# Performance work log

Measured on AMD Instinct MI355X. Metric: run time of the kernel, lower is better.

Reference implementation:

```python
import jax, jax.numpy as jnp
import numpy as np

N, L2, C = 4096, 49, 128   # lmax=6 -> (lmax+1)**2 = 49
RES = 18                   # grid resolution (beta, alpha)


def setup_inputs() -> dict:
    key = jax.random.key(0)
    k1, k2, k3 = jax.random.split(key, 3)
    inputs = jax.random.normal(k1, (N, L2, C), dtype=jnp.float32)
    # Stand-ins for the precomputed spherical-harmonic transform matrices
    # (to_grid_mat / from_grid_mat), shape (res_beta, res_alpha, (lmax+1)**2).
    W_to = jax.random.normal(k2, (RES, RES, L2), dtype=jnp.float32) / jnp.sqrt(jnp.float32(L2))
    W_from = jax.random.normal(k3, (RES, RES, L2), dtype=jnp.float32) / jnp.sqrt(jnp.float32(RES * RES))
    return {"inputs": inputs, "W_to": W_to, "W_from": W_from}


def reference(inputs, W_to, W_from):
    # to_grid: coefficients -> real-space S2 grid  (n, beta, alpha, c)
    grid = jnp.einsum('bai,nic->nbac', W_to, inputs)
    # elementwise self tensor product on the grid
    grid = grid * grid
    # from_grid: project back to spherical-harmonic coefficients (n, i, c)
    outputs = jnp.einsum('bai,nbac->nic', W_from, grid)
    return outputs
```

## Files before the change

### kernel.cpp

```cpp
#include <hip/hip_runtime.h>


#define NN    4096
#define L2D   49
#define CCH   128
#define GTOT  324
#define MT1P  22
#define KC2   11

typedef __attribute__((ext_vector_type(8))) short bf16x8;
typedef __attribute__((ext_vector_type(4))) float f32x4;

#define WT_SHORTS (MT1P * 2 * 64 * 8)
#define WF_SHORTS (4 * KC2 * 64 * 8)
#define W_SHORTS  (WT_SHORTS + WF_SHORTS)

__device__ __forceinline__ short f2bf(float f) {
    union { float f; unsigned u; } x; x.f = f;
    return (short)((x.u + 0x7fffu + ((x.u >> 16) & 1u)) >> 16);
}

__device__ __forceinline__ unsigned cvtpk(float lo, float hi) {
    unsigned r;
    asm("v_cvt_pk_bf16_f32 %0, %1, %2" : "=v"(r) : "v"(lo), "v"(hi));
    return r;
}

__global__ void prep_w_kernel(const float* __restrict__ Wt,
                              const float* __restrict__ Wf,
                              short* __restrict__ WtF,
                              short* __restrict__ WfF)
{
    int idx = blockIdx.x * 256 + threadIdx.x;
    if (idx < WT_SHORTS) {
        int j = idx & 7, lane = (idx >> 3) & 63, kcx = (idx >> 9) & 1, mt = idx >> 10;
        int g = mt * 16 + (lane & 15);
        int i = kcx * 32 + (lane >> 4) * 8 + j;
        WtF[idx] = f2bf((g < GTOT && i < L2D) ? Wt[g * L2D + i] : 0.0f);
    } else if (idx < WT_SHORTS + WF_SHORTS) {
        int e = idx - WT_SHORTS;
        int j = e & 7, lane = (e >> 3) & 63, t = e >> 9;
        int kc2 = t % KC2, it = t / KC2;
        int i = it * 16 + (lane & 15);
        int g = kc2 * 32 + (j >> 2) * 16 + (lane >> 4) * 4 + (j & 3);
        WfF[e] = f2bf((g < GTOT && i < L2D) ? Wf[g * L2D + i] : 0.0f);
    }
}

__global__ __launch_bounds__(1024, 4)
void stp_mfma3_kernel(const float* __restrict__ inp,
                      const short* __restrict__ Wbase,
                      float* __restrict__ out)
{
    __shared__ __attribute__((aligned(16))) short sW[W_SHORTS];

    const int tid = threadIdx.x;

    {
        const uint4* __restrict__ src = (const uint4*)Wbase;
        uint4* dst = (uint4*)sW;
        #pragma unroll
        for (int e = 0; e < 6; ++e) {
            int idx = tid + e * 1024;
            if (idx < W_SHORTS / 8) dst[idx] = src[idx];
        }
    }
    __syncthreads();

    const int lane = tid & 63;
    const int wave = tid >> 6;
    const int lm   = lane & 15;
    const int quad = lane >> 4;
    const int q    = wave & 3;
    const int nw   = wave >> 2;

    const short* sWt = sW;
    const short* sWf = sW + WT_SHORTS;

    for (int rep = 0; rep < 4; ++rep) {
        const int n = blockIdx.x * 16 + rep * 4 + nw;
        const float* __restrict__ Xn = inp + (size_t)n * (L2D * CCH);

        bf16x8 Bx[2][2];
        #pragma unroll
        for (int t = 0; t < 2; ++t) {
            const int c = q * 32 + t * 16 + lm;
            #pragma unroll
            for (int kcx = 0; kcx < 2; ++kcx) {
                union { bf16x8 v; unsigned u[4]; } b;
                #pragma unroll
                for (int p = 0; p < 4; ++p) {
                    const int i0 = kcx * 32 + quad * 8 + 2 * p;
                    float v0 = (i0     < L2D) ? Xn[(i0    ) * CCH + c] : 0.0f;
                    float v1 = (i0 + 1 < L2D) ? Xn[(i0 + 1) * CCH + c] : 0.0f;
                    b.u[p] = cvtpk(v0, v1);
                }
                Bx[t][kcx] = b.v;
            }
        }

        f32x4 acc2[4][2];
        #pragma unroll
        for (int it = 0; it < 4; ++it)
            #pragma unroll
            for (int t = 0; t < 2; ++t)
                acc2[it][t] = (f32x4){0.0f, 0.0f, 0.0f, 0.0f};

        #pragma unroll 1
        for (int kc2 = 0; kc2 < KC2; ++kc2) {
            bf16x8 Wtf[2][2];
            #pragma unroll
            for (int tt = 0; tt < 2; ++tt)
                #pragma unroll
                for (int kcx = 0; kcx < 2; ++kcx)
                    Wtf[tt][kcx] = *(const bf16x8*)&sWt[(((2 * kc2 + tt) * 2 + kcx) * 64 + lane) * 8];
            bf16x8 Wff[4];
            #pragma unroll
            for (int it = 0; it < 4; ++it)
                Wff[it] = *(const bf16x8*)&sWf[((it * KC2 + kc2) * 64 + lane) * 8];

            #pragma unroll
            for (int t = 0; t < 2; ++t) {
                union { bf16x8 v; unsigned u[4]; } bg;
                #pragma unroll
                for (int tt = 0; tt < 2; ++tt) {
                    f32x4 g = (f32x4){0.0f, 0.0f, 0.0f, 0.0f};
                    g = __builtin_amdgcn_mfma_f32_16x16x32_bf16(Wtf[tt][0], Bx[t][0], g, 0, 0, 0);
                    g = __builtin_amdgcn_mfma_f32_16x16x32_bf16(Wtf[tt][1], Bx[t][1], g, 0, 0, 0);
                    bg.u[tt * 2 + 0] = cvtpk(g[0] * g[0], g[1] * g[1]);
                    bg.u[tt * 2 + 1] = cvtpk(g[2] * g[2], g[3] * g[3]);
                }
                #pragma unroll
                for (int it = 0; it < 4; ++it)
                    acc2[it][t] = __builtin_amdgcn_mfma_f32_16x16x32_bf16(Wff[it], bg.v, acc2[it][t], 0, 0, 0);
            }
        }

        float* __restrict__ On = out + (size_t)n * (L2D * CCH);
        #pragma unroll
        for (int it = 0; it < 4; ++it) {
            #pragma unroll
            for (int t = 0; t < 2; ++t) {
                const int c = q * 32 + t * 16 + lm;
                #pragma unroll
                for (int r = 0; r < 4; ++r) {
                    const int i = it * 16 + quad * 4 + r;
                    if (i < L2D) On[i * CCH + c] = acc2[it][t][r];
                }
            }
        }
    }
}

extern "C" void kernel_launch(void* const* d_in, const int* in_sizes, int n_in,
                              void* d_out, int out_size, void* d_ws, size_t ws_size,
                              hipStream_t stream) {
    const float* inp = (const float*)d_in[0];
    const float* Wt  = (const float*)d_in[1];
    const float* Wf  = (const float*)d_in[2];
    float* out = (float*)d_out;

    short* WtF = (short*)d_ws;
    short* WfF = WtF + WT_SHORTS;

    const int prep_threads = WT_SHORTS + WF_SHORTS;
    prep_w_kernel<<<(prep_threads + 255) / 256, 256, 0, stream>>>(Wt, Wf, WtF, WfF);
    stp_mfma3_kernel<<<256, 1024, 0, stream>>>(inp, (const short*)WtF, out);
}
```

Baseline: 232.0 us.

## Drop LDS weight staging and launch one small block per sample

Replaces the 256-block, 1024-thread kernel, which staged the bf16 weight fragments in shared memory and looped over 4 sample reps, with 4096 blocks of 256 threads. Each wave now handles one (sample, channel-quarter) task and reads weight fragments straight from global memory, relying on L1/L2 caching. This removes the block-wide LDS copy, the barrier and the serial rep loop, and gives better load balance across CUs. The cost is repeated global/L2 weight reads per wave in the inner loop instead of LDS reads.

Result: no change. 231.2 us (-0.3%).

```diff
diff --git a/kernel.cpp b/kernel.cpp
--- a/kernel.cpp
+++ b/kernel.cpp
@@ -13,7 +13,6 @@
 
 #define WT_SHORTS (MT1P * 2 * 64 * 8)
 #define WF_SHORTS (4 * KC2 * 64 * 8)
-#define W_SHORTS  (WT_SHORTS + WF_SHORTS)
 
 __device__ __forceinline__ short f2bf(float f) {
     union { float f; unsigned u; } x; x.f = f;
@@ -47,106 +46,89 @@
     }
 }
 
-__global__ __launch_bounds__(1024, 4)
-void stp_mfma3_kernel(const float* __restrict__ inp,
-                      const short* __restrict__ Wbase,
+__global__ __launch_bounds__(256, 4)
+void stp_mfma6_kernel(const float* __restrict__ inp,
+                      const short* __restrict__ WtF,
+                      const short* __restrict__ WfF,
                       float* __restrict__ out)
 {
-    __shared__ __attribute__((aligned(16))) short sW[W_SHORTS];
-
-    const int tid = threadIdx.x;
-
-    {
-        const uint4* __restrict__ src = (const uint4*)Wbase;
-        uint4* dst = (uint4*)sW;
-        #pragma unroll
-        for (int e = 0; e < 6; ++e) {
-            int idx = tid + e * 1024;
-            if (idx < W_SHORTS / 8) dst[idx] = src[idx];
-        }
-    }
-    __syncthreads();
-
+    const int tid  = threadIdx.x;
     const int lane = tid & 63;
     const int wave = tid >> 6;
     const int lm   = lane & 15;
     const int quad = lane >> 4;
-    const int q    = wave & 3;
-    const int nw   = wave >> 2;
 
-    const short* sWt = sW;
-    const short* sWf = sW + WT_SHORTS;
+    const int task = blockIdx.x * 4 + wave;
+    const int n    = task >> 2;
+    const int q    = task & 3;
 
-    for (int rep = 0; rep < 4; ++rep) {
-        const int n = blockIdx.x * 16 + rep * 4 + nw;
-        const float* __restrict__ Xn = inp + (size_t)n * (L2D * CCH);
+    const float* __restrict__ Xn = inp + (size_t)n * (L2D * CCH);
 
-        bf16x8 Bx[2][2];
+    bf16x8 Bx[2][2];
+    #pragma unroll
+    for (int t = 0; t < 2; ++t) {
+        const int c = q * 32 + t * 16 + lm;
+        #pragma unroll
+        for (int kcx = 0; kcx < 2; ++kcx) {
+            union { bf16x8 v; unsigned u[4]; } b;
+            #pragma unroll
+            for (int p = 0; p < 4; ++p) {
+                const int i0 = kcx * 32 + quad * 8 + 2 * p;
+                float v0 = (i0     < L2D) ? Xn[(i0    ) * CCH + c] : 0.0f;
+                float v1 = (i0 + 1 < L2D) ? Xn[(i0 + 1) * CCH + c] : 0.0f;
+                b.u[p] = cvtpk(v0, v1);
+            }
+            Bx[t][kcx] = b.v;
+        }
+    }
+
+    f32x4 acc2[4][2];
+    #pragma unroll
+    for (int it = 0; it < 4; ++it)
+        #pragma unroll
+        for (int t = 0; t < 2; ++t)
+            acc2[it][t] = (f32x4){0.0f, 0.0f, 0.0f, 0.0f};
+
+    #pragma unroll 1
+    for (int kc2 = 0; kc2 < KC2; ++kc2) {
+        bf16x8 Wtf[2][2];
+        #pragma unroll
+        for (int tt = 0; tt < 2; ++tt)
+            #pragma unroll
+            for (int kcx = 0; kcx < 2; ++kcx)
+                Wtf[tt][kcx] = *(const bf16x8*)&WtF[(((2 * kc2 + tt) * 2 + kcx) * 64 + lane) * 8];
+        bf16x8 Wff[4];
+        #pragma unroll
+        for (int it = 0; it < 4; ++it)
+            Wff[it] = *(const bf16x8*)&WfF[((it * KC2 + kc2) * 64 + lane) * 8];
+
+        #pragma unroll
+        for (int t = 0; t < 2; ++t) {
+            union { bf16x8 v; unsigned u[4]; } bg;
+            #pragma unroll
+            for (int tt = 0; tt < 2; ++tt) {
+                f32x4 g = (f32x4){0.0f, 0.0f, 0.0f, 0.0f};
+                g = __builtin_amdgcn_mfma_f32_16x16x32_bf16(Wtf[tt][0], Bx[t][0], g, 0, 0, 0);
+                g = __builtin_amdgcn_mfma_f32_16x16x32_bf16(Wtf[tt][1], Bx[t][1], g, 0, 0, 0);
+                bg.u[tt * 2 + 0] = cvtpk(g[0] * g[0], g[1] * g[1]);
+                bg.u[tt * 2 + 1] = cvtpk(g[2] * g[2], g[3] * g[3]);
+            }
+            #pragma unroll
+            for (int it = 0; it < 4; ++it)
+                acc2[it][t] = __builtin_amdgcn_mfma_f32_16x16x32_bf16(Wff[it], bg.v, acc2[it][t], 0, 0, 0);
+        }
+    }
+
+    float* __restrict__ On = out + (size_t)n * (L2D * CCH);
+    #pragma unroll
+    for (int it = 0; it < 4; ++it) {
         #pragma unroll
         for (int t = 0; t < 2; ++t) {
             const int c = q * 32 + t * 16 + lm;
             #pragma unroll
-            for (int kcx = 0; kcx < 2; ++kcx) {
-                union { bf16x8 v; unsigned u[4]; } b;
-                #pragma unroll
-                for (int p = 0; p < 4; ++p) {
-                    const int i0 = kcx * 32 + quad * 8 + 2 * p;
-                    float v0 = (i0     < L2D) ? Xn[(i0    ) * CCH + c] : 0.0f;
-                    float v1 = (i0 + 1 < L2D) ? Xn[(i0 + 1) * CCH + c] : 0.0f;
-                    b.u[p] = cvtpk(v0, v1);
-                }
-                Bx[t][kcx] = b.v;
-            }
-        }
-
-        f32x4 acc2[4][2];
-        #pragma unroll
-        for (int it = 0; it < 4; ++it)
-            #pragma unroll
-            for (int t = 0; t < 2; ++t)
-                acc2[it][t] = (f32x4){0.0f, 0.0f, 0.0f, 0.0f};
-
-        #pragma unroll 1
-        for (int kc2 = 0; kc2 < KC2; ++kc2) {
-            bf16x8 Wtf[2][2];
-            #pragma unroll
-            for (int tt = 0; tt < 2; ++tt)
-                #pragma unroll
-                for (int kcx = 0; kcx < 2; ++kcx)
-                    Wtf[tt][kcx] = *(const bf16x8*)&sWt[(((2 * kc2 + tt) * 2 + kcx) * 64 + lane) * 8];
-            bf16x8 Wff[4];
-            #pragma unroll
-            for (int it = 0; it < 4; ++it)
-                Wff[it] = *(const bf16x8*)&sWf[((it * KC2 + kc2) * 64 + lane) * 8];
-
-            #pragma unroll
-            for (int t = 0; t < 2; ++t) {
-                union { bf16x8 v; unsigned u[4]; } bg;
-                #pragma unroll
-                for (int tt = 0; tt < 2; ++tt) {
-                    f32x4 g = (f32x4){0.0f, 0.0f, 0.0f, 0.0f};
-                    g = __builtin_amdgcn_mfma_f32_16x16x32_bf16(Wtf[tt][0], Bx[t][0], g, 0, 0, 0);
-                    g = __builtin_amdgcn_mfma_f32_16x16x32_bf16(Wtf[tt][1], Bx[t][1], g, 0, 0, 0);
-                    bg.u[tt * 2 + 0] = cvtpk(g[0] * g[0], g[1] * g[1]);
-                    bg.u[tt * 2 + 1] = cvtpk(g[2] * g[2], g[3] * g[3]);
-                }
-                #pragma unroll
-                for (int it = 0; it < 4; ++it)
-                    acc2[it][t] = __builtin_amdgcn_mfma_f32_16x16x32_bf16(Wff[it], bg.v, acc2[it][t], 0, 0, 0);
-            }
-        }
-
-        float* __restrict__ On = out + (size_t)n * (L2D * CCH);
-        #pragma unroll
-        for (int it = 0; it < 4; ++it) {
-            #pragma unroll
-            for (int t = 0; t < 2; ++t) {
-                const int c = q * 32 + t * 16 + lm;
-                #pragma unroll
-                for (int r = 0; r < 4; ++r) {
-                    const int i = it * 16 + quad * 4 + r;
-                    if (i < L2D) On[i * CCH + c] = acc2[it][t][r];
-                }
+            for (int r = 0; r < 4; ++r) {
+                const int i = it * 16 + quad * 4 + r;
+                if (i < L2D) On[i * CCH + c] = acc2[it][t][r];
             }
         }
     }
@@ -165,5 +147,5 @@
 
     const int prep_threads = WT_SHORTS + WF_SHORTS;
     prep_w_kernel<<<(prep_threads + 255) / 256, 256, 0, stream>>>(Wt, Wf, WtF, WfF);
-    stp_mfma3_kernel<<<256, 1024, 0, stream>>>(inp, (const short*)WtF, out);
+    stp_mfma6_kernel<<<4096, 256, 0, stream>>>(inp, WtF, WfF, out);
 }
```
